# Kernel tuning notes

Measured on AMD Instinct MI355X. Metric: run time of the kernel, lower is better.

## Reference

```python
import jax, jax.numpy as jnp
import numpy as np


def setup_inputs() -> dict:
    key = jax.random.key(0)
    k1, k2, k3, k4 = jax.random.split(key, 4)
    B, T, F, U = 64, 1024, 256, 512
    x = jax.random.normal(k1, (B, T, F), dtype=jnp.float32)
    # small init scale keeps the linear-activation cell state numerically tame
    kernel = jax.random.normal(k2, (F, 4 * U), dtype=jnp.float32) * 0.05
    recurrent_kernel = jax.random.normal(k3, (U, 4 * U), dtype=jnp.float32) * 0.05
    bias = jax.random.normal(k4, (4 * U,), dtype=jnp.float32) * 0.05
    return {"x": x, "kernel": kernel, "recurrent_kernel": recurrent_kernel, "bias": bias}


def reference(x, kernel, recurrent_kernel, bias):
    # Keras LSTM with activation=None (linear candidate / linear output),
    # recurrent_activation=sigmoid, gate order [i, f, c, o]; then external tanh.
    B, T, F = x.shape
    U = recurrent_kernel.shape[0]
    # precompute input projections for all timesteps: [T, B, 4U]
    xz = jnp.einsum('btf,fg->tbg', x, kernel) + bias

    def step(carry, xz_t):
        h, c = carry
        z = xz_t + h @ recurrent_kernel  # [B, 4U]
        i, f, g, o = jnp.split(z, 4, axis=-1)
        i = jax.nn.sigmoid(i)
        f = jax.nn.sigmoid(f)
        o = jax.nn.sigmoid(o)
        c = f * c + i * g          # candidate activation is linear (None)
        h = o * c                  # output activation is linear (None)
        return (h, c), h

    h0 = jnp.zeros((B, U), dtype=x.dtype)
    c0 = jnp.zeros((B, U), dtype=x.dtype)
    (_, _), hs = jax.lax.scan(step, (h0, c0), xz)  # hs: [T, B, U]
    seq = jnp.swapaxes(hs, 0, 1)  # [B, T, U] (return_sequences=True)
    return jnp.tanh(seq)          # external activation applied post-hoc
```

## Files before the change

kernel.cpp:

```cpp
#include <hip/hip_runtime.h>
#include <stdint.h>


#define Tt   1024
#define Uu   512
#define G4U  2048
#define NWG  256
#define NTHR 128
#define TAGSTRIDE 16

#define WF_ELEMS (2 * 24 * 64 * 8)
#define WF_BYTES (WF_ELEMS * 2)
#define ZB_PLANE (16 * 17)
#define ZB_HALF  (4 * ZB_PLANE)
#define SMEM_BYTES (WF_BYTES + 2 * ZB_HALF * 4)

typedef short  bf16x8 __attribute__((ext_vector_type(8)));
typedef float  f32x4  __attribute__((ext_vector_type(4)));
typedef int    int4v  __attribute__((ext_vector_type(4)));
typedef unsigned int u32;

__device__ __forceinline__ unsigned short f2bf(float f) {
  u32 u = __builtin_bit_cast(u32, f);
  u += 0x7fffu + ((u >> 16) & 1u);
  return (unsigned short)(u >> 16);
}

__device__ __forceinline__ int4v ld16_ag(const unsigned short* p) {
  int4v r;
  asm volatile("global_load_dwordx4 %0, %1, off sc1"
               : "=v"(r) : "v"(p) : "memory");
  return r;
}
__device__ __forceinline__ int4v ld16_nc(const float* p) {
  int4v r;
  asm volatile("global_load_dwordx4 %0, %1, off"
               : "=v"(r) : "v"(p) : "memory");
  return r;
}
__device__ __forceinline__ void store2_ag(unsigned short* p, unsigned short v) {
  asm volatile("global_store_short %0, %1, off sc1"
               :: "v"(p), "v"((u32)v) : "memory");
}
__device__ __forceinline__ void store4_ag(u32* p, u32 v) {
  asm volatile("global_store_dword %0, %1, off sc1"
               :: "v"(p), "v"(v) : "memory");
}

__device__ __forceinline__ float sigf(float z) {
  return __builtin_amdgcn_rcpf(1.f + __expf(-z));
}
__device__ __forceinline__ float tanh_fast(float v) {
  const float e = __expf(-2.f * fabsf(v));
  const float r = (1.f - e) * __builtin_amdgcn_rcpf(1.f + e);
  return copysignf(r, v);
}

extern "C" __global__ void __launch_bounds__(NTHR, 1)
lstm_persistent(const float* __restrict__ x,
                const float* __restrict__ Wk,
                const float* __restrict__ Rk,
                const float* __restrict__ bias,
                float* __restrict__ out,
                unsigned short* __restrict__ hbuf,
                u32* __restrict__ tags)
{
  extern __shared__ char smem[];
  unsigned short* wf   = (unsigned short*)smem;
  float*          zbuf = (float*)(smem + WF_BYTES);

  const int bid = blockIdx.x;
  const int tid = threadIdx.x;
  const int w   = tid >> 6;
  const int l   = tid & 63;
  const int g   = bid & 3;
  const int m   = bid >> 2;

  for (int i = tid; i < WF_ELEMS; i += NTHR) {
    const int j    = i & 7;
    const int lane = (i >> 3) & 63;
    const int kt   = (i >> 9) % 24;
    const int nt   = (i >> 9) / 24;
    const int k    = kt * 32 + ((lane >> 4) << 3) + j;
    const int n    = nt * 16 + (lane & 15);
    const int zc   = (n >> 3) * Uu + m * 8 + (n & 7);
    const float v  = (k < 256) ? Wk[(size_t)k * G4U + zc]
                               : Rk[(size_t)(k - 256) * G4U + zc];
    wf[i] = f2bf(v);
  }
  __syncthreads();

  bf16x8 wfx[4][2];
  #pragma unroll
  for (int q = 0; q < 4; ++q)
    #pragma unroll
    for (int nt = 0; nt < 2; ++nt)
      wfx[q][nt] = *(const bf16x8*)(wf + (((nt * 24) + (2 * q + w)) * 64 + l) * 8);

  const int row_c = tid >> 3;
  const int uu    = tid & 7;
  const int b_out = g * 16 + row_c;
  const int u_out = m * 8 + uu;
  float breg[4];
  #pragma unroll
  for (int gg = 0; gg < 4; ++gg) breg[gg] = bias[gg * Uu + u_out];
  float creg = 0.f;

  const int b_ld = g * 16 + (l & 15);
  const int kq   = (l >> 4) * 8;
  const u32* tagp = tags + ((size_t)g * 64 + l) * TAGSTRIDE;

  int4v xv[4][2];
  {
    const float* xp0 = x + ((size_t)b_ld * Tt + 0) * 256 + kq;
    #pragma unroll
    for (int q = 0; q < 4; ++q) {
      const int kt = 2 * q + w;
      xv[q][0] = ld16_nc(xp0 + kt * 32);
      xv[q][1] = ld16_nc(xp0 + kt * 32 + 4);
    }
  }
  u32 tv = 0;
  if (w == 0)
    asm volatile("global_load_dword %0, %1, off sc1"
                 : "=v"(tv) : "v"(tagp) : "memory");
  asm volatile("s_waitcnt vmcnt(0)" ::: "memory");
  __builtin_amdgcn_sched_barrier(0);

  for (int t = 0; t < Tt; ++t) {
    f32x4 aX0 = {0.f, 0.f, 0.f, 0.f};
    f32x4 aX1 = {0.f, 0.f, 0.f, 0.f};
    #pragma unroll
    for (int q = 0; q < 4; ++q) {
      const f32x4 v0 = __builtin_bit_cast(f32x4, xv[q][0]);
      const f32x4 v1 = __builtin_bit_cast(f32x4, xv[q][1]);
      int r0, r1, r2, r3;
      asm("v_cvt_pk_bf16_f32 %0, %1, %2" : "=v"(r0) : "v"(v0[0]), "v"(v0[1]));
      asm("v_cvt_pk_bf16_f32 %0, %1, %2" : "=v"(r1) : "v"(v0[2]), "v"(v0[3]));
      asm("v_cvt_pk_bf16_f32 %0, %1, %2" : "=v"(r2) : "v"(v1[0]), "v"(v1[1]));
      asm("v_cvt_pk_bf16_f32 %0, %1, %2" : "=v"(r3) : "v"(v1[2]), "v"(v1[3]));
      const int4v ai = {r0, r1, r2, r3};
      const bf16x8 a = __builtin_bit_cast(bf16x8, ai);
      aX0 = __builtin_amdgcn_mfma_f32_16x16x32_bf16(a, wfx[q][0], aX0, 0, 0, 0);
      aX1 = __builtin_amdgcn_mfma_f32_16x16x32_bf16(a, wfx[q][1], aX1, 0, 0, 0);
    }

    if (w == 0) {
      asm volatile("s_waitcnt vmcnt(1)" ::: "memory");
      __builtin_amdgcn_sched_barrier(0);
      while (!__all(tv >= (u32)t)) {
        __builtin_amdgcn_s_sleep(1);
        asm volatile("global_load_dword %0, %1, off sc1\n\ts_waitcnt vmcnt(0)"
                     : "=v"(tv) : "v"(tagp) : "memory");
        __builtin_amdgcn_sched_barrier(0);
      }
    }
    __builtin_amdgcn_s_barrier();
    __builtin_amdgcn_sched_barrier(0);

    const unsigned short* hrow =
        hbuf + ((size_t)(t & 1) * 64 + b_ld) * Uu + kq;
    int4v hf[8];
    #pragma unroll
    for (int q = 0; q < 8; ++q)
      hf[q] = ld16_ag(hrow + (2 * q + w) * 32);
    {
      const int tn = (t + 1 < Tt) ? t + 1 : t;
      const float* xpn = x + ((size_t)b_ld * Tt + tn) * 256 + kq;
      #pragma unroll
      for (int q = 0; q < 4; ++q) {
        const int kt = 2 * q + w;
        xv[q][0] = ld16_nc(xpn + kt * 32);
        xv[q][1] = ld16_nc(xpn + kt * 32 + 4);
      }
    }

    f32x4 aH0 = {0.f, 0.f, 0.f, 0.f};
    f32x4 aH1 = {0.f, 0.f, 0.f, 0.f};
    asm volatile("s_waitcnt vmcnt(12)" ::: "memory");
    __builtin_amdgcn_sched_barrier(0);
    #pragma unroll
    for (int q = 0; q < 4; ++q) {
      const int kt = 8 + 2 * q + w;
      const bf16x8 a = __builtin_bit_cast(bf16x8, hf[q]);
      const bf16x8 b0 = *(const bf16x8*)(wf + ((0 * 24 + kt) * 64 + l) * 8);
      const bf16x8 b1 = *(const bf16x8*)(wf + ((1 * 24 + kt) * 64 + l) * 8);
      aH0 = __builtin_amdgcn_mfma_f32_16x16x32_bf16(a, b0, aH0, 0, 0, 0);
      aH1 = __builtin_amdgcn_mfma_f32_16x16x32_bf16(a, b1, aH1, 0, 0, 0);
    }
    asm volatile("s_waitcnt vmcnt(8)" ::: "memory");
    __builtin_amdgcn_sched_barrier(0);
    #pragma unroll
    for (int q = 4; q < 8; ++q) {
      const int kt = 8 + 2 * q + w;
      const bf16x8 a = __builtin_bit_cast(bf16x8, hf[q]);
      const bf16x8 b0 = *(const bf16x8*)(wf + ((0 * 24 + kt) * 64 + l) * 8);
      const bf16x8 b1 = *(const bf16x8*)(wf + ((1 * 24 + kt) * 64 + l) * 8);
      aH0 = __builtin_amdgcn_mfma_f32_16x16x32_bf16(a, b0, aH0, 0, 0, 0);
      aH1 = __builtin_amdgcn_mfma_f32_16x16x32_bf16(a, b1, aH1, 0, 0, 0);
    }

    const f32x4 z0 = aX0 + aH0;
    const f32x4 z1 = aX1 + aH1;

    float* zb = zbuf + (t & 1) * ZB_HALF;
    {
      float* zw = zb + ((w * 2 + 0) * 16 + (l >> 4) * 4) * 17 + (l & 15);
      #pragma unroll
      for (int r = 0; r < 4; ++r) {
        zw[r * 17]           = z0[r];
        zw[r * 17 + 16 * 17] = z1[r];
      }
    }
    __syncthreads();

    float z[4];
    #pragma unroll
    for (int gg = 0; gg < 4; ++gg) {
      const int n  = gg * 8 + uu;
      const int nt = n >> 4, nc = n & 15;
      z[gg] = zb[((0 + nt) * 16 + row_c) * 17 + nc]
            + zb[((2 + nt) * 16 + row_c) * 17 + nc]
            + breg[gg];
    }
    const float ig = sigf(z[0]);
    const float fg = sigf(z[1]);
    const float og = sigf(z[3]);
    const float cc = fg * creg + ig * z[2];
    creg = cc;
    const float hh = og * cc;

    store2_ag(hbuf + ((size_t)((t + 1) & 1) * 64 + b_out) * Uu + u_out,
              f2bf(hh));
    asm volatile("s_waitcnt vmcnt(0)" ::: "memory");
    __builtin_amdgcn_sched_barrier(0);
    __builtin_amdgcn_s_barrier();
    __builtin_amdgcn_sched_barrier(0);
    if (tid == 0)
      store4_ag(tags + ((size_t)g * 64 + m) * TAGSTRIDE, (u32)(t + 1));
    if (w == 0)
      asm volatile("global_load_dword %0, %1, off sc1"
                   : "=v"(tv) : "v"(tagp) : "memory");
    {
      const float ov = tanh_fast(hh);
      float* op = out + ((size_t)b_out * Tt + t) * Uu + u_out;
      asm volatile("global_store_dword %0, %1, off nt"
                   :: "v"(op), "v"(ov) : "memory");
    }
  }
}

extern "C" void kernel_launch(void* const* d_in, const int* in_sizes, int n_in,
                              void* d_out, int out_size, void* d_ws, size_t ws_size,
                              hipStream_t stream) {
  const float* x    = (const float*)d_in[0];
  const float* Wk   = (const float*)d_in[1];
  const float* Rk   = (const float*)d_in[2];
  const float* bias = (const float*)d_in[3];
  float* out = (float*)d_out;
  unsigned short* hbuf = (unsigned short*)d_ws;
  u32* tags = (u32*)((char*)d_ws + (size_t)2 * 64 * Uu * sizeof(unsigned short));

  (void)hipMemsetAsync(d_ws, 0,
                       (size_t)2 * 64 * Uu * sizeof(unsigned short)
                         + (size_t)4 * 64 * TAGSTRIDE * sizeof(u32),
                       stream);

  (void)hipFuncSetAttribute((const void*)lstm_persistent,
                            hipFuncAttributeMaxDynamicSharedMemorySize,
                            SMEM_BYTES);

  hipLaunchKernelGGL(lstm_persistent, dim3(NWG), dim3(NTHR), SMEM_BYTES, stream,
                     x, Wk, Rk, bias, out, hbuf, tags);
}
```

Measured before the change: 2.753 ms.

## Embed step tags in packed hidden-state words and validate loaded h per element

The hidden-state buffer changes from bf16 to 32-bit words that carry the bf16 value in the low half and the step index in the high half. Each reader loads twice as many bytes and spins until every word it reads carries the expected step tag, then repacks the halves into bf16 vectors for the MFMA. The existing per-workgroup tag polling and barrier are kept, so the per-element check is redundant with it. The change doubles h traffic, adds min-reduction and perm ALU work, and drops the split-waitcnt overlap between h loads and MFMAs.

After: 3.174 ms. 1.15x slower.

```diff
diff --git a/kernel.cpp b/kernel.cpp
--- a/kernel.cpp
+++ b/kernel.cpp
@@ -25,8 +25,9 @@
   u += 0x7fffu + ((u >> 16) & 1u);
   return (unsigned short)(u >> 16);
 }
-
-__device__ __forceinline__ int4v ld16_ag(const unsigned short* p) {
+__device__ __forceinline__ u32 umin32(u32 a, u32 b) { return a < b ? a : b; }
+
+__device__ __forceinline__ int4v ld16_ag(const u32* p) {
   int4v r;
   asm volatile("global_load_dwordx4 %0, %1, off sc1"
                : "=v"(r) : "v"(p) : "memory");
@@ -37,10 +38,6 @@
   asm volatile("global_load_dwordx4 %0, %1, off"
                : "=v"(r) : "v"(p) : "memory");
   return r;
-}
-__device__ __forceinline__ void store2_ag(unsigned short* p, unsigned short v) {
-  asm volatile("global_store_short %0, %1, off sc1"
-               :: "v"(p), "v"((u32)v) : "memory");
 }
 __device__ __forceinline__ void store4_ag(u32* p, u32 v) {
   asm volatile("global_store_dword %0, %1, off sc1"
@@ -62,7 +59,7 @@
                 const float* __restrict__ Rk,
                 const float* __restrict__ bias,
                 float* __restrict__ out,
-                unsigned short* __restrict__ hbuf,
+                u32* __restrict__ hbuf,
                 u32* __restrict__ tags)
 {
   extern __shared__ char smem[];
@@ -158,12 +155,13 @@
     __builtin_amdgcn_s_barrier();
     __builtin_amdgcn_sched_barrier(0);
 
-    const unsigned short* hrow =
-        hbuf + ((size_t)(t & 1) * 64 + b_ld) * Uu + kq;
-    int4v hf[8];
-    #pragma unroll
-    for (int q = 0; q < 8; ++q)
-      hf[q] = ld16_ag(hrow + (2 * q + w) * 32);
+    const u32* hp = hbuf + ((size_t)(t & 1) * 64 + b_ld) * Uu + kq;
+    int4v hf[16];
+    #pragma unroll
+    for (int q = 0; q < 8; ++q) {
+      hf[2 * q]     = ld16_ag(hp + (2 * q + w) * 32);
+      hf[2 * q + 1] = ld16_ag(hp + (2 * q + w) * 32 + 4);
+    }
     {
       const int tn = (t + 1 < Tt) ? t + 1 : t;
       const float* xpn = x + ((size_t)b_ld * Tt + tn) * 256 + kq;
@@ -175,25 +173,40 @@
       }
     }
 
+    asm volatile("s_waitcnt vmcnt(8)" ::: "memory");
+    __builtin_amdgcn_sched_barrier(0);
+    for (;;) {
+      u32 m0 = ~0u, m1 = ~0u, m2 = ~0u, m3 = ~0u;
+      #pragma unroll
+      for (int q = 0; q < 16; ++q) {
+        m0 = umin32(m0, (u32)hf[q][0]);
+        m1 = umin32(m1, (u32)hf[q][1]);
+        m2 = umin32(m2, (u32)hf[q][2]);
+        m3 = umin32(m3, (u32)hf[q][3]);
+      }
+      const u32 mv = umin32(umin32(m0, m1), umin32(m2, m3));
+      if (__all((mv >> 16) == (u32)t)) break;
+      __builtin_amdgcn_s_sleep(1);
+      #pragma unroll
+      for (int q = 0; q < 8; ++q) {
+        hf[2 * q]     = ld16_ag(hp + (2 * q + w) * 32);
+        hf[2 * q + 1] = ld16_ag(hp + (2 * q + w) * 32 + 4);
+      }
+      asm volatile("s_waitcnt vmcnt(0)" ::: "memory");
+      __builtin_amdgcn_sched_barrier(0);
+    }
+
     f32x4 aH0 = {0.f, 0.f, 0.f, 0.f};
     f32x4 aH1 = {0.f, 0.f, 0.f, 0.f};
-    asm volatile("s_waitcnt vmcnt(12)" ::: "memory");
-    __builtin_amdgcn_sched_barrier(0);
-    #pragma unroll
-    for (int q = 0; q < 4; ++q) {
+    #pragma unroll
+    for (int q = 0; q < 8; ++q) {
       const int kt = 8 + 2 * q + w;
-      const bf16x8 a = __builtin_bit_cast(bf16x8, hf[q]);
-      const bf16x8 b0 = *(const bf16x8*)(wf + ((0 * 24 + kt) * 64 + l) * 8);
-      const bf16x8 b1 = *(const bf16x8*)(wf + ((1 * 24 + kt) * 64 + l) * 8);
-      aH0 = __builtin_amdgcn_mfma_f32_16x16x32_bf16(a, b0, aH0, 0, 0, 0);
-      aH1 = __builtin_amdgcn_mfma_f32_16x16x32_bf16(a, b1, aH1, 0, 0, 0);
-    }
-    asm volatile("s_waitcnt vmcnt(8)" ::: "memory");
-    __builtin_amdgcn_sched_barrier(0);
-    #pragma unroll
-    for (int q = 4; q < 8; ++q) {
-      const int kt = 8 + 2 * q + w;
-      const bf16x8 a = __builtin_bit_cast(bf16x8, hf[q]);
+      const u32 w0_ = __builtin_amdgcn_perm((u32)hf[2*q][1],   (u32)hf[2*q][0],   0x05040100u);
+      const u32 w1_ = __builtin_amdgcn_perm((u32)hf[2*q][3],   (u32)hf[2*q][2],   0x05040100u);
+      const u32 w2_ = __builtin_amdgcn_perm((u32)hf[2*q+1][1], (u32)hf[2*q+1][0], 0x05040100u);
+      const u32 w3_ = __builtin_amdgcn_perm((u32)hf[2*q+1][3], (u32)hf[2*q+1][2], 0x05040100u);
+      const int4v ai = {(int)w0_, (int)w1_, (int)w2_, (int)w3_};
+      const bf16x8 a = __builtin_bit_cast(bf16x8, ai);
       const bf16x8 b0 = *(const bf16x8*)(wf + ((0 * 24 + kt) * 64 + l) * 8);
       const bf16x8 b1 = *(const bf16x8*)(wf + ((1 * 24 + kt) * 64 + l) * 8);
       aH0 = __builtin_amdgcn_mfma_f32_16x16x32_bf16(a, b0, aH0, 0, 0, 0);
@@ -230,10 +243,10 @@
     creg = cc;
     const float hh = og * cc;
 
-    store2_ag(hbuf + ((size_t)((t + 1) & 1) * 64 + b_out) * Uu + u_out,
-              f2bf(hh));
     asm volatile("s_waitcnt vmcnt(0)" ::: "memory");
     __builtin_amdgcn_sched_barrier(0);
+    const u32 hw = ((u32)(t + 1) << 16) | (u32)f2bf(hh);
+    store4_ag(hbuf + ((size_t)((t + 1) & 1) * 64 + b_out) * Uu + u_out, hw);
     __builtin_amdgcn_s_barrier();
     __builtin_amdgcn_sched_barrier(0);
     if (tid == 0)
@@ -258,11 +271,11 @@
   const float* Rk   = (const float*)d_in[2];
   const float* bias = (const float*)d_in[3];
   float* out = (float*)d_out;
-  unsigned short* hbuf = (unsigned short*)d_ws;
-  u32* tags = (u32*)((char*)d_ws + (size_t)2 * 64 * Uu * sizeof(unsigned short));
+  u32* hbuf = (u32*)d_ws;
+  u32* tags = (u32*)((char*)d_ws + (size_t)2 * 64 * Uu * sizeof(u32));
 
   (void)hipMemsetAsync(d_ws, 0,
-                       (size_t)2 * 64 * Uu * sizeof(unsigned short)
+                       (size_t)2 * 64 * Uu * sizeof(u32)
                          + (size_t)4 * 64 * TAGSTRIDE * sizeof(u32),
                        stream);
 
```

## Split gate columns across wavefronts to drop LDS z-exchange and block barrier

Applied to the files above, without the earlier changes.

Before, each wavefront handled half of the K dimension for all 32 gate columns, so partial sums had to be combined through LDS with a __syncthreads. Now each wavefront owns 4 unit columns for all four gates and covers the full K range. The weight layout is permuted so that i/f/c/o for a unit land in lanes a shuffle apart, and the gate combine becomes cross-lane __shfl with no LDS round trip and no extra barrier. In exchange each wave issues twice as many h and x loads and a longer dependent MFMA chain, and only a quarter of the lanes do the stores.

New measurement: 3.948 ms. 43.4% more time.

```diff
diff --git a/kernel.cpp b/kernel.cpp
--- a/kernel.cpp
+++ b/kernel.cpp
@@ -11,9 +11,7 @@
 
 #define WF_ELEMS (2 * 24 * 64 * 8)
 #define WF_BYTES (WF_ELEMS * 2)
-#define ZB_PLANE (16 * 17)
-#define ZB_HALF  (4 * ZB_PLANE)
-#define SMEM_BYTES (WF_BYTES + 2 * ZB_HALF * 4)
+#define SMEM_BYTES WF_BYTES
 
 typedef short  bf16x8 __attribute__((ext_vector_type(8)));
 typedef float  f32x4  __attribute__((ext_vector_type(4)));
@@ -66,8 +64,7 @@
                 u32* __restrict__ tags)
 {
   extern __shared__ char smem[];
-  unsigned short* wf   = (unsigned short*)smem;
-  float*          zbuf = (float*)(smem + WF_BYTES);
+  unsigned short* wf = (unsigned short*)smem;
 
   const int bid = blockIdx.x;
   const int tid = threadIdx.x;
@@ -80,44 +77,40 @@
     const int j    = i & 7;
     const int lane = (i >> 3) & 63;
     const int kt   = (i >> 9) % 24;
-    const int nt   = (i >> 9) / 24;
+    const int tau  = (i >> 9) / 24;
     const int k    = kt * 32 + ((lane >> 4) << 3) + j;
-    const int n    = nt * 16 + (lane & 15);
-    const int zc   = (n >> 3) * Uu + m * 8 + (n & 7);
+    const int n    = lane & 15;
+    const int zc   = (n >> 2) * Uu + m * 8 + tau * 4 + (n & 3);
     const float v  = (k < 256) ? Wk[(size_t)k * G4U + zc]
                                : Rk[(size_t)(k - 256) * G4U + zc];
     wf[i] = f2bf(v);
   }
   __syncthreads();
 
-  bf16x8 wfx[4][2];
+  bf16x8 wfx[8];
   #pragma unroll
-  for (int q = 0; q < 4; ++q)
-    #pragma unroll
-    for (int nt = 0; nt < 2; ++nt)
-      wfx[q][nt] = *(const bf16x8*)(wf + (((nt * 24) + (2 * q + w)) * 64 + l) * 8);
-
-  const int row_c = tid >> 3;
-  const int uu    = tid & 7;
-  const int b_out = g * 16 + row_c;
-  const int u_out = m * 8 + uu;
-  float breg[4];
-  #pragma unroll
-  for (int gg = 0; gg < 4; ++gg) breg[gg] = bias[gg * Uu + u_out];
-  float creg = 0.f;
-
-  const int b_ld = g * 16 + (l & 15);
+  for (int q = 0; q < 8; ++q)
+    wfx[q] = *(const bf16x8*)(wf + ((w * 24 + q) * 64 + l) * 8);
+
+  const int n15   = l & 15;
+  const float blane = bias[(n15 >> 2) * Uu + m * 8 + w * 4 + (n15 & 3)];
+  const int sbase = (l & 48) + (l & 3);
+  const bool gm   = (n15 < 4);
+  const int u_out = m * 8 + w * 4 + (l & 3);
+  const int b_row0 = g * 16 + (l >> 4) * 4;
+  float creg[4] = {0.f, 0.f, 0.f, 0.f};
+
+  const int b_ld = g * 16 + n15;
   const int kq   = (l >> 4) * 8;
   const u32* tagp = tags + ((size_t)g * 64 + l) * TAGSTRIDE;
 
-  int4v xv[4][2];
+  int4v xv[8][2];
   {
-    const float* xp0 = x + ((size_t)b_ld * Tt + 0) * 256 + kq;
-    #pragma unroll
-    for (int q = 0; q < 4; ++q) {
-      const int kt = 2 * q + w;
-      xv[q][0] = ld16_nc(xp0 + kt * 32);
-      xv[q][1] = ld16_nc(xp0 + kt * 32 + 4);
+    const float* xp0 = x + (size_t)b_ld * Tt * 256 + kq;
+    #pragma unroll
+    for (int q = 0; q < 8; ++q) {
+      xv[q][0] = ld16_nc(xp0 + q * 32);
+      xv[q][1] = ld16_nc(xp0 + q * 32 + 4);
     }
   }
   u32 tv = 0;
@@ -128,10 +121,9 @@
   __builtin_amdgcn_sched_barrier(0);
 
   for (int t = 0; t < Tt; ++t) {
-    f32x4 aX0 = {0.f, 0.f, 0.f, 0.f};
-    f32x4 aX1 = {0.f, 0.f, 0.f, 0.f};
-    #pragma unroll
-    for (int q = 0; q < 4; ++q) {
+    f32x4 acc = {0.f, 0.f, 0.f, 0.f};
+    #pragma unroll
+    for (int q = 0; q < 8; ++q) {
       const f32x4 v0 = __builtin_bit_cast(f32x4, xv[q][0]);
       const f32x4 v1 = __builtin_bit_cast(f32x4, xv[q][1]);
       int r0, r1, r2, r3;
@@ -141,12 +133,11 @@
       asm("v_cvt_pk_bf16_f32 %0, %1, %2" : "=v"(r3) : "v"(v1[2]), "v"(v1[3]));
       const int4v ai = {r0, r1, r2, r3};
       const bf16x8 a = __builtin_bit_cast(bf16x8, ai);
-      aX0 = __builtin_amdgcn_mfma_f32_16x16x32_bf16(a, wfx[q][0], aX0, 0, 0, 0);
-      aX1 = __builtin_amdgcn_mfma_f32_16x16x32_bf16(a, wfx[q][1], aX1, 0, 0, 0);
+      acc = __builtin_amdgcn_mfma_f32_16x16x32_bf16(a, wfx[q], acc, 0, 0, 0);
     }
 
     if (w == 0) {
-      asm volatile("s_waitcnt vmcnt(1)" ::: "memory");
+      asm volatile("s_waitcnt vmcnt(4)" ::: "memory");
       __builtin_amdgcn_sched_barrier(0);
       while (!__all(tv >= (u32)t)) {
         __builtin_amdgcn_s_sleep(1);
@@ -160,78 +151,63 @@
 
     const unsigned short* hrow =
         hbuf + ((size_t)(t & 1) * 64 + b_ld) * Uu + kq;
-    int4v hf[8];
-    #pragma unroll
-    for (int q = 0; q < 8; ++q)
-      hf[q] = ld16_ag(hrow + (2 * q + w) * 32);
+    int4v hf[16];
+    #pragma unroll
+    for (int q = 0; q < 16; ++q)
+      hf[q] = ld16_ag(hrow + q * 32);
     {
       const int tn = (t + 1 < Tt) ? t + 1 : t;
       const float* xpn = x + ((size_t)b_ld * Tt + tn) * 256 + kq;
       #pragma unroll
-      for (int q = 0; q < 4; ++q) {
-        const int kt = 2 * q + w;
-        xv[q][0] = ld16_nc(xpn + kt * 32);
-        xv[q][1] = ld16_nc(xpn + kt * 32 + 4);
-      }
-    }
-
-    f32x4 aH0 = {0.f, 0.f, 0.f, 0.f};
-    f32x4 aH1 = {0.f, 0.f, 0.f, 0.f};
-    asm volatile("s_waitcnt vmcnt(12)" ::: "memory");
-    __builtin_amdgcn_sched_barrier(0);
-    #pragma unroll
-    for (int q = 0; q < 4; ++q) {
-      const int kt = 8 + 2 * q + w;
+      for (int q = 0; q < 8; ++q) {
+        xv[q][0] = ld16_nc(xpn + q * 32);
+        xv[q][1] = ld16_nc(xpn + q * 32 + 4);
+      }
+    }
+
+    asm volatile("s_waitcnt vmcnt(24)" ::: "memory");
+    __builtin_amdgcn_sched_barrier(0);
+    #pragma unroll
+    for (int q = 0; q < 8; ++q) {
       const bf16x8 a = __builtin_bit_cast(bf16x8, hf[q]);
-      const bf16x8 b0 = *(const bf16x8*)(wf + ((0 * 24 + kt) * 64 + l) * 8);
-      const bf16x8 b1 = *(const bf16x8*)(wf + ((1 * 24 + kt) * 64 + l) * 8);
-      aH0 = __builtin_amdgcn_mfma_f32_16x16x32_bf16(a, b0, aH0, 0, 0, 0);
-      aH1 = __builtin_amdgcn_mfma_f32_16x16x32_bf16(a, b1, aH1, 0, 0, 0);
-    }
-    asm volatile("s_waitcnt vmcnt(8)" ::: "memory");
-    __builtin_amdgcn_sched_barrier(0);
-    #pragma unroll
-    for (int q = 4; q < 8; ++q) {
-      const int kt = 8 + 2 * q + w;
+      const bf16x8 b = *(const bf16x8*)(wf + ((w * 24 + 8 + q) * 64 + l) * 8);
+      acc = __builtin_amdgcn_mfma_f32_16x16x32_bf16(a, b, acc, 0, 0, 0);
+    }
+    asm volatile("s_waitcnt vmcnt(16)" ::: "memory");
+    __builtin_amdgcn_sched_barrier(0);
+    #pragma unroll
+    for (int q = 8; q < 16; ++q) {
       const bf16x8 a = __builtin_bit_cast(bf16x8, hf[q]);
-      const bf16x8 b0 = *(const bf16x8*)(wf + ((0 * 24 + kt) * 64 + l) * 8);
-      const bf16x8 b1 = *(const bf16x8*)(wf + ((1 * 24 + kt) * 64 + l) * 8);
-      aH0 = __builtin_amdgcn_mfma_f32_16x16x32_bf16(a, b0, aH0, 0, 0, 0);
-      aH1 = __builtin_amdgcn_mfma_f32_16x16x32_bf16(a, b1, aH1, 0, 0, 0);
-    }
-
-    const f32x4 z0 = aX0 + aH0;
-    const f32x4 z1 = aX1 + aH1;
-
-    float* zb = zbuf + (t & 1) * ZB_HALF;
+      const bf16x8 b = *(const bf16x8*)(wf + ((w * 24 + 8 + q) * 64 + l) * 8);
+      acc = __builtin_amdgcn_mfma_f32_16x16x32_bf16(a, b, acc, 0, 0, 0);
+    }
+
+    float hv[4];
     {
-      float* zw = zb + ((w * 2 + 0) * 16 + (l >> 4) * 4) * 17 + (l & 15);
+      f32x4 zv;
+      #pragma unroll
+      for (int r = 0; r < 4; ++r) zv[r] = acc[r] + blane;
       #pragma unroll
       for (int r = 0; r < 4; ++r) {
-        zw[r * 17]           = z0[r];
-        zw[r * 17 + 16 * 17] = z1[r];
-      }
-    }
-    __syncthreads();
-
-    float z[4];
-    #pragma unroll
-    for (int gg = 0; gg < 4; ++gg) {
-      const int n  = gg * 8 + uu;
-      const int nt = n >> 4, nc = n & 15;
-      z[gg] = zb[((0 + nt) * 16 + row_c) * 17 + nc]
-            + zb[((2 + nt) * 16 + row_c) * 17 + nc]
-            + breg[gg];
-    }
-    const float ig = sigf(z[0]);
-    const float fg = sigf(z[1]);
-    const float og = sigf(z[3]);
-    const float cc = fg * creg + ig * z[2];
-    creg = cc;
-    const float hh = og * cc;
-
-    store2_ag(hbuf + ((size_t)((t + 1) & 1) * 64 + b_out) * Uu + u_out,
-              f2bf(hh));
+        const float zi = __shfl(zv[r], sbase + 0, 64);
+        const float zf = __shfl(zv[r], sbase + 4, 64);
+        const float zc = __shfl(zv[r], sbase + 8, 64);
+        const float zo = __shfl(zv[r], sbase + 12, 64);
+        const float ig = sigf(zi);
+        const float fg = sigf(zf);
+        const float og = sigf(zo);
+        const float cc = fg * creg[r] + ig * zc;
+        creg[r] = cc;
+        hv[r] = og * cc;
+      }
+    }
+
+    if (gm) {
+      #pragma unroll
+      for (int r = 0; r < 4; ++r)
+        store2_ag(hbuf + ((size_t)(((t + 1) & 1)) * 64 + b_row0 + r) * Uu
+                       + u_out, f2bf(hv[r]));
+    }
     asm volatile("s_waitcnt vmcnt(0)" ::: "memory");
     __builtin_amdgcn_sched_barrier(0);
     __builtin_amdgcn_s_barrier();
@@ -241,11 +217,14 @@
     if (w == 0)
       asm volatile("global_load_dword %0, %1, off sc1"
                    : "=v"(tv) : "v"(tagp) : "memory");
-    {
-      const float ov = tanh_fast(hh);
-      float* op = out + ((size_t)b_out * Tt + t) * Uu + u_out;
-      asm volatile("global_store_dword %0, %1, off nt"
-                   :: "v"(op), "v"(ov) : "memory");
+    if (gm) {
+      #pragma unroll
+      for (int r = 0; r < 4; ++r) {
+        const float ov = tanh_fast(hv[r]);
+        float* op = out + ((size_t)(b_row0 + r) * Tt + t) * Uu + u_out;
+        asm volatile("global_store_dword %0, %1, off nt"
+                     :: "v"(op), "v"(ov) : "memory");
+      }
     }
   }
 }
```
